# Kernel tuning notes

Hardware: AMD Instinct MI355X
Metric: run time of the kernel (lower is better)

Reference implementation:

```python
import jax, jax.numpy as jnp
import numpy as np

B, H, S, D = 4, 16, 2048, 128


def setup_inputs() -> dict:
    key = jax.random.key(0)
    kq, kk, kv = jax.random.split(key, 3)
    query = jax.random.normal(kq, (B, H, S, D), dtype=jnp.float32)
    key_t = jax.random.normal(kk, (B, H, S, D), dtype=jnp.float32)
    value = jax.random.normal(kv, (B, H, S, D), dtype=jnp.float32)
    # causal mask, broadcast over batch and heads: True = keep
    mask = jnp.tril(jnp.ones((S, S), dtype=bool))[None, None].repeat(B, 0).repeat(H, 1)
    return {"query": query, "key": key_t, "value": value, "mask": mask}


def reference(query, key, value, mask):
    scale = 1.0 / np.sqrt(D).astype(np.float32)
    # [b,h,sq,sk] scores
    scores = jnp.einsum("bhqd,bhkd->bhqk", query, key) * scale
    scores = jnp.where(mask, scores, -jnp.inf)
    probs = jax.nn.softmax(scores, axis=-1)
    return jnp.einsum("bhqk,bhkd->bhqd", probs, value)
```

## Files before the change

kernel.cpp:

```cpp
#include <hip/hip_runtime.h>


#define SLEN 2048
#define DDIM 128
#define NBH  64
#define QB   256
#define KB   64
#define NITEMS 512

typedef __bf16 bf16x8 __attribute__((ext_vector_type(8)));
typedef float  f32x16 __attribute__((ext_vector_type(16)));
typedef float  f32x4  __attribute__((ext_vector_type(4)));
typedef unsigned uint32x4 __attribute__((ext_vector_type(4)));
typedef unsigned short ushort_t;
typedef ushort_t ushort8 __attribute__((ext_vector_type(8)));

__device__ inline ushort_t f2bf(float f) {
  union { float f; unsigned u; } v; v.f = f;
  unsigned u = v.u;
  u += 0x7FFFu + ((u >> 16) & 1u);
  return (ushort_t)(u >> 16);
}

__device__ inline unsigned cvtpk_bf16(float lo, float hi) {
  unsigned r;
  asm("v_cvt_pk_bf16_f32 %0, %1, %2" : "=v"(r) : "v"(lo), "v"(hi));
  return r;
}

__device__ inline float exp2_fast(float x) {
  float r;
  asm("v_exp_f32 %0, %1" : "=v"(r) : "v"(x));
  return r;
}

__global__ __launch_bounds__(256) void prepass_kernel(
    const float* __restrict__ V, ushort_t* __restrict__ Vt,
    int* __restrict__ cnt) {
  __shared__ float t[64][33];
  if (blockIdx.x == 0 && threadIdx.x == 0) *cnt = 0;
  const int vb = (int)blockIdx.x;
  const int bh = vb >> 7;
  const int d0 = ((vb >> 5) & 3) * 32;
  const int s0 = (vb & 31) * 64;
  const int tx = threadIdx.x & 31;
  const int ty = threadIdx.x >> 5;
  const float* src = V + ((size_t)bh * SLEN + s0) * DDIM + d0;
#pragma unroll
  for (int j = 0; j < 8; ++j) {
    int sl = ty + j * 8;
    t[sl][tx] = src[(size_t)sl * DDIM + tx];
  }
  __syncthreads();
  ushort_t* dst = Vt + ((size_t)bh * DDIM + d0) * SLEN + s0;
#pragma unroll
  for (int j = 0; j < 4; ++j) {
    int dl = ty + j * 8;
    unsigned lo = f2bf(t[tx * 2][dl]);
    unsigned hi = f2bf(t[tx * 2 + 1][dl]);
    *reinterpret_cast<unsigned*>(&dst[(size_t)dl * SLEN + tx * 2]) =
        lo | (hi << 16);
  }
}

__global__ __launch_bounds__(512, 2) void fattn9_kernel(
    const float* __restrict__ Q, const float* __restrict__ Kf32,
    const ushort_t* __restrict__ Vt, float* __restrict__ Out,
    int* __restrict__ cnt) {
  __shared__ ushort_t K_sh[2][KB * DDIM];
  __shared__ ushort_t V_sh[2][DDIM * KB];
  __shared__ int item_sh;

  const int tid  = threadIdx.x;
  const int lane = tid & 63;
  const int wv   = tid >> 6;
  const int l31  = lane & 31;
  const int hi   = lane >> 5;

  const float qscale = 0.12751744f;
  const float THR = 11.0f;

  float4 kr0a, kr0b, kr1a, kr1b;
  const int kch0 = tid;
  const int kch1 = 512 + tid;
  const int krow0 = kch0 >> 4, kp0 = kch0 & 15;
  const int krow1 = kch1 >> 4, kp1 = kch1 & 15;
  const int kgc0 = kp0 ^ (krow0 & 7);
  const int kgc1 = kp1 ^ (krow1 & 7);

  while (true) {
    if (tid == 0) item_sh = atomicAdd(cnt, 1);
    __syncthreads();
    const int item = item_sh;
    if (item >= NITEMS) break;

    const int qblk = 7 - (item >> 6);
    const int bh   = item & 63;

    const float*    Qp = Q    + (size_t)bh * SLEN * DDIM;
    const float*    Kp = Kf32 + (size_t)bh * SLEN * DDIM;
    const ushort_t* Vp = Vt   + (size_t)bh * DDIM * SLEN;
    float*          Op = Out  + (size_t)bh * SLEN * DDIM;

    const int q0w = qblk * QB + wv * 32;
    const int qg  = q0w + l31;

    bf16x8 qf[8];
    {
      const float* qr = Qp + (size_t)qg * DDIM;
#pragma unroll
      for (int ds = 0; ds < 8; ++ds) {
        int d0 = ds * 16 + hi * 8;
        float4 x = *reinterpret_cast<const float4*>(qr + d0);
        float4 y = *reinterpret_cast<const float4*>(qr + d0 + 4);
        ushort8 uu;
        uu[0] = f2bf(x.x * qscale); uu[1] = f2bf(x.y * qscale);
        uu[2] = f2bf(x.z * qscale); uu[3] = f2bf(x.w * qscale);
        uu[4] = f2bf(y.x * qscale); uu[5] = f2bf(y.y * qscale);
        uu[6] = f2bf(y.z * qscale); uu[7] = f2bf(y.w * qscale);
        qf[ds] = __builtin_bit_cast(bf16x8, uu);
      }
    }

    f32x16 Oacc[4];
#pragma unroll
    for (int dt = 0; dt < 4; ++dt)
#pragma unroll
      for (int r = 0; r < 16; ++r) Oacc[dt][r] = 0.f;
    float m_run = -3.0e38f, l_run = 0.f;

    const int last_kb       = qblk * 4 + 3;
    const int last_kb_wave  = (q0w + 31) >> 6;

    auto kload = [&](int kb) {
      const float* ksrc = Kp + (size_t)kb * KB * DDIM;
      const float* g0 = ksrc + krow0 * DDIM + kgc0 * 8;
      const float* g1 = ksrc + krow1 * DDIM + kgc1 * 8;
      kr0a = *reinterpret_cast<const float4*>(g0);
      kr0b = *reinterpret_cast<const float4*>(g0 + 4);
      kr1a = *reinterpret_cast<const float4*>(g1);
      kr1b = *reinterpret_cast<const float4*>(g1 + 4);
    };
    auto kwrite = [&](int buf) {
      uint32x4 w0, w1;
      w0.x = cvtpk_bf16(kr0a.x, kr0a.y); w0.y = cvtpk_bf16(kr0a.z, kr0a.w);
      w0.z = cvtpk_bf16(kr0b.x, kr0b.y); w0.w = cvtpk_bf16(kr0b.z, kr0b.w);
      w1.x = cvtpk_bf16(kr1a.x, kr1a.y); w1.y = cvtpk_bf16(kr1a.z, kr1a.w);
      w1.z = cvtpk_bf16(kr1b.x, kr1b.y); w1.w = cvtpk_bf16(kr1b.z, kr1b.w);
      *reinterpret_cast<uint32x4*>(&K_sh[buf][krow0 * DDIM + kp0 * 8]) = w0;
      *reinterpret_cast<uint32x4*>(&K_sh[buf][krow1 * DDIM + kp1 * 8]) = w1;
    };
    auto vstage = [&](int buf, int kb) {
      const ushort_t* vsrc = Vp + (size_t)kb * KB;
#pragma unroll
      for (int j = 0; j < 2; ++j) {
        int chunk = wv * 128 + j * 64 + lane;
        int row = chunk >> 3, c = chunk & 7;
        const ushort_t* g = vsrc + (size_t)row * SLEN + ((c ^ (row & 7)) << 3);
        ushort_t* l = &V_sh[buf][(wv * 128 + j * 64) * 8];
        __builtin_amdgcn_global_load_lds(
            (const __attribute__((address_space(1))) unsigned*)g,
            (__attribute__((address_space(3))) unsigned*)l, 16, 0, 0);
      }
    };

    kload(0);
    vstage(0, 0);
    kwrite(0);
    __syncthreads();

    for (int kb = 0; kb <= last_kb; ++kb) {
      const int buf = kb & 1;
      if (kb < last_kb) {
        kload(kb + 1);
        vstage(buf ^ 1, kb + 1);
      }

      if (kb <= last_kb_wave) {
        f32x16 sac[2];
#pragma unroll
        for (int mt = 0; mt < 2; ++mt) {
          f32x16 a;
#pragma unroll
          for (int r = 0; r < 16; ++r) a[r] = 0.f;
          int row = mt * 32 + l31;
          int sw = row & 7;
          __builtin_amdgcn_s_setprio(1);
#pragma unroll
          for (int ds = 0; ds < 8; ++ds) {
            int c = ds * 2 + hi;
            bf16x8 kf = *reinterpret_cast<const bf16x8*>(
                &K_sh[buf][row * DDIM + ((c ^ sw) << 3)]);
            a = __builtin_amdgcn_mfma_f32_32x32x16_bf16(kf, qf[ds], a, 0, 0, 0);
          }
          __builtin_amdgcn_s_setprio(0);
          sac[mt] = a;
        }

        if (kb * 64 + 63 > q0w) {
#pragma unroll
          for (int mt = 0; mt < 2; ++mt) {
            int kbase = kb * 64 + mt * 32 + 4 * hi;
#pragma unroll
            for (int r = 0; r < 16; ++r) {
              int krow = (r & 3) + 8 * (r >> 2);
              if (kbase + krow > qg) sac[mt][r] = -3.0e38f;
            }
          }
        }

        float p0 = sac[0][0], p1 = sac[0][1], p2 = sac[0][2], p3 = sac[0][3];
#pragma unroll
        for (int r = 4; r < 16; r += 4) {
          p0 = fmaxf(p0, sac[0][r + 0]); p1 = fmaxf(p1, sac[0][r + 1]);
          p2 = fmaxf(p2, sac[0][r + 2]); p3 = fmaxf(p3, sac[0][r + 3]);
        }
#pragma unroll
        for (int r = 0; r < 16; r += 4) {
          p0 = fmaxf(p0, sac[1][r + 0]); p1 = fmaxf(p1, sac[1][r + 1]);
          p2 = fmaxf(p2, sac[1][r + 2]); p3 = fmaxf(p3, sac[1][r + 3]);
        }
        float tm = fmaxf(fmaxf(p0, p1), fmaxf(p2, p3));
        tm = fmaxf(tm, __shfl_xor(tm, 32));

        if (!__all(tm - m_run <= THR)) {
          float mnew  = fmaxf(m_run, tm);
          float alpha = exp2_fast(m_run - mnew);
          m_run = mnew;
          l_run *= alpha;
#pragma unroll
          for (int dt = 0; dt < 4; ++dt)
#pragma unroll
            for (int r = 0; r < 16; ++r) Oacc[dt][r] *= alpha;
        }

        float s0 = 0.f, s1 = 0.f, s2 = 0.f, s3 = 0.f;
#pragma unroll
        for (int mt = 0; mt < 2; ++mt)
#pragma unroll
          for (int r = 0; r < 16; r += 4) {
            float e0 = exp2_fast(sac[mt][r + 0] - m_run);
            float e1 = exp2_fast(sac[mt][r + 1] - m_run);
            float e2 = exp2_fast(sac[mt][r + 2] - m_run);
            float e3 = exp2_fast(sac[mt][r + 3] - m_run);
            sac[mt][r + 0] = e0; sac[mt][r + 1] = e1;
            sac[mt][r + 2] = e2; sac[mt][r + 3] = e3;
            s0 += e0; s1 += e1; s2 += e2; s3 += e3;
          }
        float rs = (s0 + s1) + (s2 + s3);
        rs += __shfl_xor(rs, 32);
        l_run += rs;

        uint32x4 pw[4];
#pragma unroll
        for (int ks = 0; ks < 4; ++ks) {
          const int mt = ks >> 1;
          const int hb = 8 * (ks & 1);
          unsigned X  = cvtpk_bf16(sac[mt][hb + 0], sac[mt][hb + 1]);
          unsigned X2 = cvtpk_bf16(sac[mt][hb + 2], sac[mt][hb + 3]);
          unsigned Y  = cvtpk_bf16(sac[mt][hb + 4], sac[mt][hb + 5]);
          unsigned Y2 = cvtpk_bf16(sac[mt][hb + 6], sac[mt][hb + 7]);
          asm("v_permlane32_swap_b32 %0, %1" : "+v"(X),  "+v"(Y));
          asm("v_permlane32_swap_b32 %0, %1" : "+v"(X2), "+v"(Y2));
          uint32x4 f; f.x = X; f.y = X2; f.z = Y; f.w = Y2;
          pw[ks] = f;
        }

#pragma unroll
        for (int dt = 0; dt < 4; ++dt) {
          int row = dt * 32 + l31;
          int sw = row & 7;
          __builtin_amdgcn_s_setprio(1);
#pragma unroll
          for (int ks = 0; ks < 4; ++ks) {
            int c = ks * 2 + hi;
            bf16x8 vf = *reinterpret_cast<const bf16x8*>(
                &V_sh[buf][row * 64 + ((c ^ sw) << 3)]);
            Oacc[dt] = __builtin_amdgcn_mfma_f32_32x32x16_bf16(
                vf, __builtin_bit_cast(bf16x8, pw[ks]), Oacc[dt], 0, 0, 0);
          }
          __builtin_amdgcn_s_setprio(0);
        }
      }

      if (kb < last_kb) kwrite(buf ^ 1);
      __syncthreads();
    }

    {
      float invl = 1.0f / l_run;
      float* orow = Op + (size_t)qg * DDIM;
#pragma unroll
      for (int dt = 0; dt < 4; ++dt)
#pragma unroll
        for (int rq = 0; rq < 4; ++rq) {
          float4 o;
          o.x = Oacc[dt][rq * 4 + 0] * invl;
          o.y = Oacc[dt][rq * 4 + 1] * invl;
          o.z = Oacc[dt][rq * 4 + 2] * invl;
          o.w = Oacc[dt][rq * 4 + 3] * invl;
          int d = dt * 32 + 8 * rq + 4 * hi;
          *reinterpret_cast<float4*>(orow + d) = o;
        }
    }
    __syncthreads();
  }
}

__global__ __launch_bounds__(256) void fattn_kernel(
    const float* __restrict__ Q, const float* __restrict__ K,
    const float* __restrict__ V, float* __restrict__ Out) {
  __shared__ ushort_t Kf_sh[64 * 128];
  __shared__ ushort_t Vf_sh[128 * 64];
  __shared__ ushort_t P_sh[4][16 * 64];

  const int tid  = threadIdx.x;
  const int lane = tid & 63;
  const int wv   = tid >> 6;
  const int l16  = lane & 15;
  const int lhi  = lane >> 4;
  const int qblk = blockIdx.x;
  const int bh   = blockIdx.y;
  const float scale = 0.08838834764831845f;

  const size_t base = (size_t)bh * SLEN * DDIM;
  const float* Qp = Q + base;
  const float* Kp = K + base;
  const float* Vp = V + base;
  float*       Op = Out + base;

  bf16x8 qf[4];
  {
    const int qrow = qblk * 64 + wv * 16 + l16;
    const float* qr = Qp + (size_t)qrow * DDIM;
#pragma unroll
    for (int dc = 0; dc < 4; ++dc) {
      int d0 = dc * 32 + lhi * 8;
      float4 x = *reinterpret_cast<const float4*>(qr + d0);
      float4 y = *reinterpret_cast<const float4*>(qr + d0 + 4);
      ushort8 uu;
      uu[0] = f2bf(x.x * scale); uu[1] = f2bf(x.y * scale);
      uu[2] = f2bf(x.z * scale); uu[3] = f2bf(x.w * scale);
      uu[4] = f2bf(y.x * scale); uu[5] = f2bf(y.y * scale);
      uu[6] = f2bf(y.z * scale); uu[7] = f2bf(y.w * scale);
      qf[dc] = __builtin_bit_cast(bf16x8, uu);
    }
  }

  f32x4 Oacc[8];
#pragma unroll
  for (int i = 0; i < 8; ++i) Oacc[i] = (f32x4){0.f, 0.f, 0.f, 0.f};
  float m_run[4], l_run[4];
#pragma unroll
  for (int r = 0; r < 4; ++r) { m_run[r] = -3.0e38f; l_run[r] = 0.f; }

  for (int kb = 0; kb <= qblk; ++kb) {
    __syncthreads();
    {
      const float* src = Kp + (size_t)kb * 64 * DDIM;
#pragma unroll
      for (int it = 0; it < 8; ++it) {
        int idx4 = it * 256 + tid;
        int r  = idx4 >> 5;
        int c4 = idx4 & 31;
        float4 x = *reinterpret_cast<const float4*>(src + r * DDIM + c4 * 4);
        unsigned lo = ((unsigned)f2bf(x.y) << 16) | f2bf(x.x);
        unsigned hh = ((unsigned)f2bf(x.w) << 16) | f2bf(x.z);
        int e = (r * 128 + c4 * 4) ^ ((r & 7) << 3);
        *reinterpret_cast<uint2*>(&Kf_sh[e]) = make_uint2(lo, hh);
      }
      const float* vs = Vp + (size_t)kb * 64 * DDIM;
#pragma unroll
      for (int it = 0; it < 8; ++it) {
        int idx4 = it * 256 + tid;
        int r  = idx4 >> 5;
        int c4 = idx4 & 31;
        float4 x = *reinterpret_cast<const float4*>(vs + r * DDIM + c4 * 4);
        int c0 = c4 * 4;
        float vals[4] = {x.x, x.y, x.z, x.w};
#pragma unroll
        for (int j = 0; j < 4; ++j) {
          int d = c0 + j;
          Vf_sh[(d * 64 + r) ^ ((d & 7) << 3)] = f2bf(vals[j]);
        }
      }
    }
    __syncthreads();

    f32x4 sacc[4];
#pragma unroll
    for (int g = 0; g < 4; ++g) {
      f32x4 acc = (f32x4){0.f, 0.f, 0.f, 0.f};
#pragma unroll
      for (int dc = 0; dc < 4; ++dc) {
        int row = g * 16 + l16;
        int e = (row * 128 + dc * 32 + lhi * 8) ^ ((row & 7) << 3);
        bf16x8 kf = *reinterpret_cast<const bf16x8*>(&Kf_sh[e]);
        acc = __builtin_amdgcn_mfma_f32_16x16x32_bf16(qf[dc], kf, acc, 0, 0, 0);
      }
      sacc[g] = acc;
    }

    if (kb == qblk) {
      int q0 = lhi * 4;
#pragma unroll
      for (int g = 0; g < 4; ++g) {
        int kcol = g * 16 + l16;
#pragma unroll
        for (int r = 0; r < 4; ++r) {
          if (kcol > wv * 16 + q0 + r) sacc[g][r] = -3.0e38f;
        }
      }
    }

    float tmax[4];
#pragma unroll
    for (int r = 0; r < 4; ++r)
      tmax[r] = fmaxf(fmaxf(sacc[0][r], sacc[1][r]),
                      fmaxf(sacc[2][r], sacc[3][r]));
#pragma unroll
    for (int x = 1; x < 16; x <<= 1) {
#pragma unroll
      for (int r = 0; r < 4; ++r)
        tmax[r] = fmaxf(tmax[r], __shfl_xor(tmax[r], x));
    }

    float alpha[4], mnew[4];
#pragma unroll
    for (int r = 0; r < 4; ++r) {
      mnew[r]  = fmaxf(m_run[r], tmax[r]);
      alpha[r] = __expf(m_run[r] - mnew[r]);
      m_run[r] = mnew[r];
    }

    float rsum[4] = {0.f, 0.f, 0.f, 0.f};
#pragma unroll
    for (int g = 0; g < 4; ++g) {
#pragma unroll
      for (int r = 0; r < 4; ++r) {
        float p = __expf(sacc[g][r] - mnew[r]);
        rsum[r] += p;
        int prow = lhi * 4 + r;
        P_sh[wv][(prow * 64 + g * 16 + l16) ^ ((prow & 7) << 3)] = f2bf(p);
      }
    }
#pragma unroll
    for (int x = 1; x < 16; x <<= 1) {
#pragma unroll
      for (int r = 0; r < 4; ++r) rsum[r] += __shfl_xor(rsum[r], x);
    }
#pragma unroll
    for (int r = 0; r < 4; ++r) l_run[r] = l_run[r] * alpha[r] + rsum[r];

#pragma unroll
    for (int dg = 0; dg < 8; ++dg)
#pragma unroll
      for (int r = 0; r < 4; ++r) Oacc[dg][r] *= alpha[r];

    bf16x8 pf[2];
#pragma unroll
    for (int kc = 0; kc < 2; ++kc) {
      int e = (l16 * 64 + kc * 32 + lhi * 8) ^ ((l16 & 7) << 3);
      pf[kc] = *reinterpret_cast<const bf16x8*>(&P_sh[wv][e]);
    }
#pragma unroll
    for (int dg = 0; dg < 8; ++dg) {
#pragma unroll
      for (int kc = 0; kc < 2; ++kc) {
        int row = dg * 16 + l16;
        int e = (row * 64 + kc * 32 + lhi * 8) ^ ((row & 7) << 3);
        bf16x8 vf = *reinterpret_cast<const bf16x8*>(&Vf_sh[e]);
        Oacc[dg] = __builtin_amdgcn_mfma_f32_16x16x32_bf16(pf[kc], vf, Oacc[dg], 0, 0, 0);
      }
    }
  }

#pragma unroll
  for (int r = 0; r < 4; ++r) {
    float inv = 1.0f / l_run[r];
    int q = qblk * 64 + wv * 16 + lhi * 4 + r;
    float* orow = Op + (size_t)q * DDIM;
#pragma unroll
    for (int dg = 0; dg < 8; ++dg)
      orow[dg * 16 + l16] = Oacc[dg][r] * inv;
  }
}

extern "C" void kernel_launch(void* const* d_in, const int* in_sizes, int n_in,
                              void* d_out, int out_size, void* d_ws, size_t ws_size,
                              hipStream_t stream) {
  const float* Q = (const float*)d_in[0];
  const float* K = (const float*)d_in[1];
  const float* V = (const float*)d_in[2];
  float* O = (float*)d_out;

  const size_t n_elem = (size_t)NBH * SLEN * DDIM;
  const size_t need   = n_elem * 2 + 64;

  if (ws_size >= need) {
    ushort_t* Vt = (ushort_t*)d_ws;
    int* cnt     = (int*)(Vt + n_elem);
    prepass_kernel<<<8192, 256, 0, stream>>>(V, Vt, cnt);
    fattn9_kernel<<<dim3(NITEMS), dim3(512), 0, stream>>>(Q, K, Vt, O, cnt);
  } else {
    fattn_kernel<<<dim3(SLEN / 64, NBH), dim3(256), 0, stream>>>(Q, K, V, O);
  }
}
```

Measured before the change: 136.5 us.

## Halve query block to 128 rows with 4-wave workgroups and persistent grid

The query tile shrinks from 256 to 128 rows, giving 1024 work items handled by 256-thread (4-wave) workgroups, and the grid becomes 512 persistent blocks pulling items from an atomic counter. Each thread now stages twice as many K and V chunks per key block, and causal bounds are recomputed for the smaller tile. The goal is finer-grained load balancing across the causal triangle and more resident workgroups per CU. In exchange, each K/V tile is reused by fewer query rows, so global traffic and synchronization per unit of work go up.

```diff
diff --git a/kernel.cpp b/kernel.cpp
--- a/kernel.cpp
+++ b/kernel.cpp
@@ -4,9 +4,9 @@
 #define SLEN 2048
 #define DDIM 128
 #define NBH  64
-#define QB   256
+#define QB   128
 #define KB   64
-#define NITEMS 512
+#define NITEMS 1024
 
 typedef __bf16 bf16x8 __attribute__((ext_vector_type(8)));
 typedef float  f32x16 __attribute__((ext_vector_type(16)));
@@ -63,7 +63,7 @@
   }
 }
 
-__global__ __launch_bounds__(512, 2) void fattn9_kernel(
+__global__ __launch_bounds__(256, 2) void fattn10_kernel(
     const float* __restrict__ Q, const float* __restrict__ Kf32,
     const ushort_t* __restrict__ Vt, float* __restrict__ Out,
     int* __restrict__ cnt) {
@@ -80,13 +80,12 @@
   const float qscale = 0.12751744f;
   const float THR = 11.0f;
 
-  float4 kr0a, kr0b, kr1a, kr1b;
-  const int kch0 = tid;
-  const int kch1 = 512 + tid;
-  const int krow0 = kch0 >> 4, kp0 = kch0 & 15;
-  const int krow1 = kch1 >> 4, kp1 = kch1 & 15;
-  const int kgc0 = kp0 ^ (krow0 & 7);
-  const int kgc1 = kp1 ^ (krow1 & 7);
+  const int kch0 = tid, kch1 = 256 + tid, kch2 = 512 + tid, kch3 = 768 + tid;
+  const int krow0 = kch0 >> 4, kp0 = kch0 & 15, kgc0 = kp0 ^ (krow0 & 7);
+  const int krow1 = kch1 >> 4, kp1 = kch1 & 15, kgc1 = kp1 ^ (krow1 & 7);
+  const int krow2 = kch2 >> 4, kp2 = kch2 & 15, kgc2 = kp2 ^ (krow2 & 7);
+  const int krow3 = kch3 >> 4, kp3 = kch3 & 15, kgc3 = kp3 ^ (krow3 & 7);
+  float4 kr0a, kr0b, kr1a, kr1b, kr2a, kr2b, kr3a, kr3b;
 
   while (true) {
     if (tid == 0) item_sh = atomicAdd(cnt, 1);
@@ -94,7 +93,7 @@
     const int item = item_sh;
     if (item >= NITEMS) break;
 
-    const int qblk = 7 - (item >> 6);
+    const int qblk = 15 - (item >> 6);
     const int bh   = item & 63;
 
     const float*    Qp = Q    + (size_t)bh * SLEN * DDIM;
@@ -129,35 +128,47 @@
       for (int r = 0; r < 16; ++r) Oacc[dt][r] = 0.f;
     float m_run = -3.0e38f, l_run = 0.f;
 
-    const int last_kb       = qblk * 4 + 3;
-    const int last_kb_wave  = (q0w + 31) >> 6;
+    const int last_kb      = qblk * 2 + 1;
+    const int last_kb_wave = 2 * qblk + (wv >> 1);
 
     auto kload = [&](int kb) {
       const float* ksrc = Kp + (size_t)kb * KB * DDIM;
       const float* g0 = ksrc + krow0 * DDIM + kgc0 * 8;
       const float* g1 = ksrc + krow1 * DDIM + kgc1 * 8;
+      const float* g2 = ksrc + krow2 * DDIM + kgc2 * 8;
+      const float* g3 = ksrc + krow3 * DDIM + kgc3 * 8;
       kr0a = *reinterpret_cast<const float4*>(g0);
       kr0b = *reinterpret_cast<const float4*>(g0 + 4);
       kr1a = *reinterpret_cast<const float4*>(g1);
       kr1b = *reinterpret_cast<const float4*>(g1 + 4);
+      kr2a = *reinterpret_cast<const float4*>(g2);
+      kr2b = *reinterpret_cast<const float4*>(g2 + 4);
+      kr3a = *reinterpret_cast<const float4*>(g3);
+      kr3b = *reinterpret_cast<const float4*>(g3 + 4);
     };
     auto kwrite = [&](int buf) {
-      uint32x4 w0, w1;
-      w0.x = cvtpk_bf16(kr0a.x, kr0a.y); w0.y = cvtpk_bf16(kr0a.z, kr0a.w);
-      w0.z = cvtpk_bf16(kr0b.x, kr0b.y); w0.w = cvtpk_bf16(kr0b.z, kr0b.w);
-      w1.x = cvtpk_bf16(kr1a.x, kr1a.y); w1.y = cvtpk_bf16(kr1a.z, kr1a.w);
-      w1.z = cvtpk_bf16(kr1b.x, kr1b.y); w1.w = cvtpk_bf16(kr1b.z, kr1b.w);
-      *reinterpret_cast<uint32x4*>(&K_sh[buf][krow0 * DDIM + kp0 * 8]) = w0;
-      *reinterpret_cast<uint32x4*>(&K_sh[buf][krow1 * DDIM + kp1 * 8]) = w1;
+      uint32x4 w;
+      w.x = cvtpk_bf16(kr0a.x, kr0a.y); w.y = cvtpk_bf16(kr0a.z, kr0a.w);
+      w.z = cvtpk_bf16(kr0b.x, kr0b.y); w.w = cvtpk_bf16(kr0b.z, kr0b.w);
+      *reinterpret_cast<uint32x4*>(&K_sh[buf][krow0 * DDIM + kp0 * 8]) = w;
+      w.x = cvtpk_bf16(kr1a.x, kr1a.y); w.y = cvtpk_bf16(kr1a.z, kr1a.w);
+      w.z = cvtpk_bf16(kr1b.x, kr1b.y); w.w = cvtpk_bf16(kr1b.z, kr1b.w);
+      *reinterpret_cast<uint32x4*>(&K_sh[buf][krow1 * DDIM + kp1 * 8]) = w;
+      w.x = cvtpk_bf16(kr2a.x, kr2a.y); w.y = cvtpk_bf16(kr2a.z, kr2a.w);
+      w.z = cvtpk_bf16(kr2b.x, kr2b.y); w.w = cvtpk_bf16(kr2b.z, kr2b.w);
+      *reinterpret_cast<uint32x4*>(&K_sh[buf][krow2 * DDIM + kp2 * 8]) = w;
+      w.x = cvtpk_bf16(kr3a.x, kr3a.y); w.y = cvtpk_bf16(kr3a.z, kr3a.w);
+      w.z = cvtpk_bf16(kr3b.x, kr3b.y); w.w = cvtpk_bf16(kr3b.z, kr3b.w);
+      *reinterpret_cast<uint32x4*>(&K_sh[buf][krow3 * DDIM + kp3 * 8]) = w;
     };
     auto vstage = [&](int buf, int kb) {
       const ushort_t* vsrc = Vp + (size_t)kb * KB;
 #pragma unroll
-      for (int j = 0; j < 2; ++j) {
-        int chunk = wv * 128 + j * 64 + lane;
+      for (int j = 0; j < 4; ++j) {
+        int chunk = wv * 256 + j * 64 + lane;
         int row = chunk >> 3, c = chunk & 7;
         const ushort_t* g = vsrc + (size_t)row * SLEN + ((c ^ (row & 7)) << 3);
-        ushort_t* l = &V_sh[buf][(wv * 128 + j * 64) * 8];
+        ushort_t* l = &V_sh[buf][(wv * 256 + j * 64) * 8];
         __builtin_amdgcn_global_load_lds(
             (const __attribute__((address_space(1))) unsigned*)g,
             (__attribute__((address_space(3))) unsigned*)l, 16, 0, 0);
@@ -501,7 +512,7 @@
     ushort_t* Vt = (ushort_t*)d_ws;
     int* cnt     = (int*)(Vt + n_elem);
     prepass_kernel<<<8192, 256, 0, stream>>>(V, Vt, cnt);
-    fattn9_kernel<<<dim3(NITEMS), dim3(512), 0, stream>>>(Q, K, Vt, O, cnt);
+    fattn10_kernel<<<dim3(512), dim3(256), 0, stream>>>(Q, K, Vt, O, cnt);
   } else {
     fattn_kernel<<<dim3(SLEN / 64, NBH), dim3(256), 0, stream>>>(Q, K, V, O);
   }
```

Result: slower. 146.4 us (+7.3%).
